# Kernel tuning notes

Hardware: AMD Instinct MI355X
Metric: run time of the kernel (lower is better)

## Reference

```python
import jax, jax.numpy as jnp
import numpy as np

N_NODES = 50000
N_EDGES = 1600000
HIDDEN = 512
LN_EPS = 1e-5


def setup_inputs() -> dict:
    key = jax.random.key(0)
    k1, k2, k3, k4 = jax.random.split(key, 4)
    label_emb = jax.random.normal(k1, (N_NODES, HIDDEN), dtype=jnp.float32)
    edge_index = jax.random.randint(k2, (2, N_EDGES), 0, N_NODES, dtype=jnp.int64)
    W = jax.random.normal(k3, (HIDDEN, HIDDEN), dtype=jnp.float32) / np.sqrt(HIDDEN)
    b = jnp.zeros((HIDDEN,), dtype=jnp.float32)
    gamma = jnp.ones((HIDDEN,), dtype=jnp.float32)
    beta = jnp.zeros((HIDDEN,), dtype=jnp.float32)
    return {"label_emb": label_emb, "edge_index": edge_index, "W": W, "b": b,
            "gamma": gamma, "beta": beta}


def _gcn_conv(x, src, dst, W, b, n_nodes):
    loops = jnp.arange(n_nodes, dtype=src.dtype)
    src_all = jnp.concatenate([src, loops])  # [E+N]
    dst_all = jnp.concatenate([dst, loops])
    ones = jnp.ones_like(dst_all, dtype=x.dtype)
    deg = jax.ops.segment_sum(ones, dst_all, num_segments=n_nodes)  # [N]
    dinv = jnp.where(deg > 0, jax.lax.rsqrt(deg), 0.0)
    norm = dinv[src_all] * dinv[dst_all]  # [E+N]
    h = x @ W  # [N, H] dense transform first (fewer FLOPs than per-edge)
    msgs = h[src_all] * norm[:, None]  # gather + per-edge scale
    out = jax.ops.segment_sum(msgs, dst_all, num_segments=n_nodes)  # scatter-add
    return out + b


def reference(label_emb, edge_index, W, b, gamma, beta):
    residual = label_emb
    src, dst = edge_index[0], edge_index[1]
    h = _gcn_conv(label_emb, src, dst, W, b, N_NODES)
    # dropout is identity at inference (training=False)
    h = residual + h
    mean = jnp.mean(h, axis=-1, keepdims=True)
    var = jnp.var(h, axis=-1, keepdims=True)
    h = (h - mean) * jax.lax.rsqrt(var + LN_EPS) * gamma + beta
    return h
```

## Files before the change

kernel.cpp:

```cpp
#include <hip/hip_runtime.h>

#define HID 512
#define CAP 128
#define BINCAP 384

typedef unsigned int uint32;
using bf16x8 = __attribute__((ext_vector_type(8))) short;
using f32x4  = __attribute__((ext_vector_type(4))) float;
using f32x2  = __attribute__((ext_vector_type(2))) float;
using u32x2  = __attribute__((ext_vector_type(2))) unsigned int;
using u32x4  = __attribute__((ext_vector_type(4))) unsigned int;
using u16x4  = __attribute__((ext_vector_type(4))) unsigned short;
using u16x8  = __attribute__((ext_vector_type(8))) unsigned short;

__device__ __forceinline__ unsigned short f2bf(float f) {
    uint32 u = __float_as_uint(f);
    uint32 r = (u + 0x7FFFu + ((u >> 16) & 1u)) >> 16;
    return (unsigned short)r;
}
__device__ __forceinline__ float bf2f(unsigned short u) {
    return __uint_as_float(((uint32)u) << 16);
}

__device__ __forceinline__ void gl_lds16(const unsigned short* g, unsigned short* l) {
    __builtin_amdgcn_global_load_lds(
        (const __attribute__((address_space(1))) void*)g,
        (__attribute__((address_space(3))) void*)l,
        16, 0, 0);
}

__global__ __launch_bounds__(256) void prep_bin(const int* __restrict__ src,
                                                const int* __restrict__ dst,
                                                int* __restrict__ bincnt,
                                                uint32* __restrict__ bins, int e,
                                                const float* __restrict__ X,
                                                unsigned short* __restrict__ Xbf,
                                                const float* __restrict__ W,
                                                unsigned short* __restrict__ Wt,
                                                int n_elems, int pad_elems,
                                                int nbb, int nbx) {
    const int bid = blockIdx.x;
    if (bid < nbb) {
        for (int i = bid * 256 + (int)threadIdx.x; i < e; i += nbb * 256) {
            int d = dst[i], s = src[i];
            int b = d >> 3;
            int p = atomicAdd(&bincnt[b], 1);
            bins[(size_t)b * BINCAP + p] = ((uint32)(d & 7) << 16) | (uint32)s;
        }
    } else if (bid < nbb + nbx) {
        int base = ((bid - nbb) * 256 + threadIdx.x) * 8;
        if (base < n_elems) {
            f32x4 a = *(const f32x4*)(X + base);
            f32x4 b = *(const f32x4*)(X + base + 4);
            u16x4 w0, w1;
            w0[0] = f2bf(a[0]); w0[1] = f2bf(a[1]); w0[2] = f2bf(a[2]); w0[3] = f2bf(a[3]);
            w1[0] = f2bf(b[0]); w1[1] = f2bf(b[1]); w1[2] = f2bf(b[2]); w1[3] = f2bf(b[3]);
            *(u16x4*)(Xbf + base) = w0;
            *(u16x4*)(Xbf + base + 4) = w1;
        } else if (base < pad_elems) {
            u16x4 z = {0, 0, 0, 0};
            *(u16x4*)(Xbf + base) = z;
            *(u16x4*)(Xbf + base + 4) = z;
        }
    } else {
        int idx = (bid - nbb - nbx) * 256 + threadIdx.x;
        if (idx < HID * HID) {
            int k = idx >> 9, n = idx & (HID - 1);
            Wt[n * HID + k] = f2bf(W[k * HID + n]);
        }
    }
}

__global__ __launch_bounds__(256) void bin2csr(const uint32* __restrict__ bins,
                                               const int* __restrict__ bincnt,
                                               unsigned short* __restrict__ csrf,
                                               int* __restrict__ fill) {
    __shared__ alignas(16) unsigned short lcs[128 * CAP];
    __shared__ int lcnt[128];
    const int b = blockIdx.x;
    for (int j = threadIdx.x; j < 128; j += 256) lcnt[j] = 0;
    __syncthreads();
    #pragma unroll
    for (int sb = 0; sb < 16; ++sb) {
        const int gb = b * 16 + sb;
        const int m = bincnt[gb];
        const uint32* be = bins + (size_t)gb * BINCAP;
        for (int i = threadIdx.x; i < m; i += 256) {
            uint32 ev = be[i];
            int ln = sb * 8 + (int)(ev >> 16);
            int p = atomicAdd(&lcnt[ln], 1);
            lcs[ln * CAP + p] = (unsigned short)(ev & 0xFFFFu);
        }
    }
    __syncthreads();
    u32x4* gout = (u32x4*)(csrf + (size_t)b * 128 * CAP);
    const u32x4* lin = (const u32x4*)lcs;
    for (int j = threadIdx.x; j < 128 * CAP / 8; j += 256) gout[j] = lin[j];
    if (threadIdx.x < 128) fill[b * 128 + threadIdx.x] = lcnt[threadIdx.x];
}

#define NWGX 4
__global__ __launch_bounds__(256) void gemm_xw(const unsigned short* __restrict__ Xbf,
                                               const unsigned short* __restrict__ Wt,
                                               const int* __restrict__ fill,
                                               unsigned char* __restrict__ hs8,
                                               int nwg) {
    __shared__ unsigned short Alds[128 * 64];
    __shared__ unsigned short Blds[128 * 64];
    const int cpx = nwg >> 3;
    const int swz = (blockIdx.x & 7) * cpx + (blockIdx.x >> 3);
    const int row_base = (swz >> 2) * 128;
    const int col_base = (swz & 3) * 128;

    const int t = threadIdx.x;
    const int lane = t & 63, wid = t >> 6;
    const int wm = wid >> 1, wn = wid & 1;

    const int srow = lane >> 3;
    const int gch  = ((lane & 7) ^ srow) * 8;
    const unsigned short* gA = Xbf + (size_t)(row_base + wid * 8 + srow) * HID + gch;
    const unsigned short* gB = Wt  + (size_t)(col_base + wid * 8 + srow) * HID + gch;
    unsigned short* lA = &Alds[wid * 512];
    unsigned short* lB = &Blds[wid * 512];

    f32x4 acc[4][4];
    #pragma unroll
    for (int m = 0; m < 4; ++m)
        #pragma unroll
        for (int n = 0; n < 4; ++n)
            acc[m][n] = (f32x4){0.f, 0.f, 0.f, 0.f};

    const int rr = lane & 15;
    const int kg8 = lane >> 4;

    for (int k0 = 0; k0 < HID; k0 += 64) {
        #pragma unroll
        for (int rd = 0; rd < 4; ++rd) {
            gl_lds16(gA + (size_t)rd * 32 * HID + k0, lA + rd * 2048);
            gl_lds16(gB + (size_t)rd * 32 * HID + k0, lB + rd * 2048);
        }
        __syncthreads();

        bf16x8 afr[4][2], bfr[4][2];
        #pragma unroll
        for (int m = 0; m < 4; ++m) {
            int row = wm * 64 + m * 16 + rr;
            #pragma unroll
            for (int ks = 0; ks < 2; ++ks)
                afr[m][ks] = *(const bf16x8*)&Alds[row * 64 + (((ks * 4 + kg8) ^ (row & 7)) * 8)];
        }
        #pragma unroll
        for (int n = 0; n < 4; ++n) {
            int row = wn * 64 + n * 16 + rr;
            #pragma unroll
            for (int ks = 0; ks < 2; ++ks)
                bfr[n][ks] = *(const bf16x8*)&Blds[row * 64 + (((ks * 4 + kg8) ^ (row & 7)) * 8)];
        }
        #pragma unroll
        for (int ks = 0; ks < 2; ++ks)
            #pragma unroll
            for (int m = 0; m < 4; ++m)
                #pragma unroll
                for (int n = 0; n < 4; ++n)
                    acc[m][n] = __builtin_amdgcn_mfma_f32_16x16x32_bf16(afr[m][ks], bfr[n][ks], acc[m][n], 0, 0, 0);
        __syncthreads();
    }

    const int rgrp = (lane >> 4) * 4;
    const int cc = lane & 15;
    #pragma unroll
    for (int m = 0; m < 4; ++m) {
        #pragma unroll
        for (int r = 0; r < 4; ++r) {
            int grow = row_base + wm * 64 + m * 16 + rgrp + r;
            float g = rsqrtf((float)fill[grow] + 1.0f);
            #pragma unroll
            for (int n = 0; n < 4; ++n) {
                int gcol = col_base + wn * 64 + n * 16 + cc;
                float v = acc[m][n][r] * g;
                unsigned int p = __builtin_amdgcn_cvt_pk_fp8_f32(v, v, 0u, false);
                hs8[(size_t)grow * HID + gcol] = (unsigned char)p;
            }
        }
    }
}

__device__ __forceinline__ void dec8(u32x2 v, float* acc) {
    f32x2 a = __builtin_amdgcn_cvt_pk_f32_fp8(v[0], false);
    f32x2 b = __builtin_amdgcn_cvt_pk_f32_fp8(v[0], true);
    f32x2 c = __builtin_amdgcn_cvt_pk_f32_fp8(v[1], false);
    f32x2 d = __builtin_amdgcn_cvt_pk_f32_fp8(v[1], true);
    acc[0] += a[0]; acc[1] += a[1]; acc[2] += b[0]; acc[3] += b[1];
    acc[4] += c[0]; acc[5] += c[1]; acc[6] += d[0]; acc[7] += d[1];
}

__global__ __launch_bounds__(256) void agg_ln(const unsigned char* __restrict__ hs8,
                                              const float* __restrict__ resid,
                                              const float* __restrict__ bvec,
                                              const float* __restrict__ gamma,
                                              const float* __restrict__ beta,
                                              const int* __restrict__ fill,
                                              const unsigned short* __restrict__ csrf,
                                              float* __restrict__ out, int nn) {
    const int wave = threadIdx.x >> 6;
    const int lane = threadIdx.x & 63;
    const int n = blockIdx.x * 4 + wave;
    if (n >= nn) return;
    const int c0 = lane * 8;

    float acc[8];
    #pragma unroll
    for (int j = 0; j < 8; ++j) acc[j] = 0.f;
    dec8(*(const u32x2*)(hs8 + (size_t)n * HID + c0), acc);

    const int m = fill[n];
    const unsigned short* idx = csrf + (size_t)n * CAP;
    int i = 0;
    for (; i + 8 <= m; i += 8) {
        u16x8 iv = *(const u16x8*)(idx + i);
        u32x2 v0 = *(const u32x2*)(hs8 + (size_t)iv[0] * HID + c0);
        u32x2 v1 = *(const u32x2*)(hs8 + (size_t)iv[1] * HID + c0);
        u32x2 v2 = *(const u32x2*)(hs8 + (size_t)iv[2] * HID + c0);
        u32x2 v3 = *(const u32x2*)(hs8 + (size_t)iv[3] * HID + c0);
        u32x2 v4 = *(const u32x2*)(hs8 + (size_t)iv[4] * HID + c0);
        u32x2 v5 = *(const u32x2*)(hs8 + (size_t)iv[5] * HID + c0);
        u32x2 v6 = *(const u32x2*)(hs8 + (size_t)iv[6] * HID + c0);
        u32x2 v7 = *(const u32x2*)(hs8 + (size_t)iv[7] * HID + c0);
        dec8(v0, acc); dec8(v1, acc); dec8(v2, acc); dec8(v3, acc);
        dec8(v4, acc); dec8(v5, acc); dec8(v6, acc); dec8(v7, acc);
    }
    for (; i < m; ++i)
        dec8(*(const u32x2*)(hs8 + (size_t)idx[i] * HID + c0), acc);

    const float g = rsqrtf((float)m + 1.0f);
    f32x4 r0 = __builtin_nontemporal_load((const f32x4*)(resid + (size_t)n * HID + c0));
    f32x4 r1 = __builtin_nontemporal_load((const f32x4*)(resid + (size_t)n * HID + c0 + 4));
    float val[8];
    #pragma unroll
    for (int j = 0; j < 4; ++j) {
        val[j]     = r0[j] + g * acc[j]     + bvec[c0 + j];
        val[j + 4] = r1[j] + g * acc[j + 4] + bvec[c0 + j + 4];
    }

    float s = 0.f, q = 0.f;
    #pragma unroll
    for (int j = 0; j < 8; ++j) { s += val[j]; q += val[j] * val[j]; }
    #pragma unroll
    for (int off = 32; off > 0; off >>= 1) {
        s += __shfl_xor(s, off, 64);
        q += __shfl_xor(q, off, 64);
    }
    const float mean = s * (1.f / 512.f);
    const float var = q * (1.f / 512.f) - mean * mean;
    const float rstd = rsqrtf(var + 1e-5f);

    f32x4 o0, o1;
    #pragma unroll
    for (int j = 0; j < 4; ++j) {
        o0[j] = (val[j]     - mean) * rstd * gamma[c0 + j]     + beta[c0 + j];
        o1[j] = (val[j + 4] - mean) * rstd * gamma[c0 + j + 4] + beta[c0 + j + 4];
    }
    __builtin_nontemporal_store(o0, (f32x4*)(out + (size_t)n * HID + c0));
    __builtin_nontemporal_store(o1, (f32x4*)(out + (size_t)n * HID + c0 + 4));
}

extern "C" void kernel_launch(void* const* d_in, const int* in_sizes, int n_in,
                              void* d_out, int out_size, void* d_ws, size_t ws_size,
                              hipStream_t stream) {
    const float* X     = (const float*)d_in[0];
    const int*   edges = (const int*)d_in[1];
    const float* W     = (const float*)d_in[2];
    const float* b     = (const float*)d_in[3];
    const float* gamma = (const float*)d_in[4];
    const float* beta  = (const float*)d_in[5];
    float* out = (float*)d_out;

    const int E = in_sizes[1] / 2;
    const int N = in_sizes[0] / HID;
    const int M_pad = ((N + 255) / 256) * 256;
    const int nslices = M_pad / 128;
    const int nbins = M_pad / 8;
    const int* src = edges;
    const int* dst = edges + E;

    char* w = (char*)d_ws;
    auto alloc = [&](size_t bytes) { char* p = w; w += (bytes + 255) & ~(size_t)255; return p; };
    int*    fill   = (int*)alloc((size_t)M_pad * 4);
    int*    bincnt = (int*)alloc((size_t)nbins * 4);
    uint32* bins   = (uint32*)alloc((size_t)nbins * BINCAP * 4);
    unsigned short* csrf = (unsigned short*)alloc((size_t)M_pad * CAP * 2);
    unsigned short* Wt   = (unsigned short*)alloc((size_t)HID * HID * 2);
    unsigned char*  hs8  = (unsigned char*)alloc((size_t)M_pad * HID);
    unsigned short* Xbf = (unsigned short*)d_out;

    hipMemsetAsync(bincnt, 0, (size_t)nbins * 4, stream);

    const int pad_elems = M_pad * HID;
    const int nbb = 2048;
    const int nbx = (pad_elems / 8 + 255) / 256;
    const int nbw = (HID * HID + 255) / 256;
    prep_bin<<<nbb + nbx + nbw, 256, 0, stream>>>(src, dst, bincnt, bins, E,
                                                  X, Xbf, W, Wt,
                                                  N * HID, pad_elems, nbb, nbx);

    bin2csr<<<nslices, 256, 0, stream>>>(bins, bincnt, csrf, fill);

    const int nwg = (M_pad / 128) * NWGX;
    gemm_xw<<<nwg, 256, 0, stream>>>(Xbf, Wt, fill, hs8, nwg);

    agg_ln<<<(N + 3) / 4, 256, 0, stream>>>(hs8, X, b, gamma, beta, fill, csrf, out, N);
}
```

Baseline: 285.6 us.

## Merge CSR build and GEMM into one launch, move source scaling to aggregation

Runs the bin-to-CSR blocks and the XW GEMM blocks in a single kernel launch, so the two independent stages can overlap and one launch gap disappears. Because the GEMM no longer waits for the degree counts, the source-side D^-1/2 scaling moves out of the GEMM epilogue. The aggregation instead multiplies each gathered row by a precomputed per-node dinv array. This adds one scalar gather per edge plus extra multiplies in the aggregation loop. It also changes fp8 quantization, since the unscaled products are now stored.

```diff
diff --git a/kernel.cpp b/kernel.cpp
--- a/kernel.cpp
+++ b/kernel.cpp
@@ -71,44 +71,53 @@
     }
 }
 
-__global__ __launch_bounds__(256) void bin2csr(const uint32* __restrict__ bins,
-                                               const int* __restrict__ bincnt,
-                                               unsigned short* __restrict__ csrf,
-                                               int* __restrict__ fill) {
-    __shared__ alignas(16) unsigned short lcs[128 * CAP];
-    __shared__ int lcnt[128];
-    const int b = blockIdx.x;
-    for (int j = threadIdx.x; j < 128; j += 256) lcnt[j] = 0;
-    __syncthreads();
-    #pragma unroll
-    for (int sb = 0; sb < 16; ++sb) {
-        const int gb = b * 16 + sb;
-        const int m = bincnt[gb];
-        const uint32* be = bins + (size_t)gb * BINCAP;
-        for (int i = threadIdx.x; i < m; i += 256) {
-            uint32 ev = be[i];
-            int ln = sb * 8 + (int)(ev >> 16);
-            int p = atomicAdd(&lcnt[ln], 1);
-            lcs[ln * CAP + p] = (unsigned short)(ev & 0xFFFFu);
-        }
-    }
-    __syncthreads();
-    u32x4* gout = (u32x4*)(csrf + (size_t)b * 128 * CAP);
-    const u32x4* lin = (const u32x4*)lcs;
-    for (int j = threadIdx.x; j < 128 * CAP / 8; j += 256) gout[j] = lin[j];
-    if (threadIdx.x < 128) fill[b * 128 + threadIdx.x] = lcnt[threadIdx.x];
-}
-
 #define NWGX 4
-__global__ __launch_bounds__(256) void gemm_xw(const unsigned short* __restrict__ Xbf,
-                                               const unsigned short* __restrict__ Wt,
-                                               const int* __restrict__ fill,
-                                               unsigned char* __restrict__ hs8,
-                                               int nwg) {
-    __shared__ unsigned short Alds[128 * 64];
-    __shared__ unsigned short Blds[128 * 64];
+__global__ __launch_bounds__(256) void csr_gemm(const uint32* __restrict__ bins,
+                                                const int* __restrict__ bincnt,
+                                                unsigned short* __restrict__ csrf,
+                                                int* __restrict__ fill,
+                                                float* __restrict__ dinvf,
+                                                const unsigned short* __restrict__ Xbf,
+                                                const unsigned short* __restrict__ Wt,
+                                                unsigned char* __restrict__ hs8,
+                                                int nslices, int nwg) {
+    __shared__ alignas(16) unsigned char smem[128 * CAP * 2 + 128 * 4];
+
+    if ((int)blockIdx.x < nslices) {
+        unsigned short* lcs = (unsigned short*)smem;
+        int* lcnt = (int*)(smem + 128 * CAP * 2);
+        const int b = blockIdx.x;
+        for (int j = threadIdx.x; j < 128; j += 256) lcnt[j] = 0;
+        __syncthreads();
+        #pragma unroll
+        for (int sb = 0; sb < 16; ++sb) {
+            const int gb = b * 16 + sb;
+            const int m = bincnt[gb];
+            const uint32* be = bins + (size_t)gb * BINCAP;
+            for (int i = threadIdx.x; i < m; i += 256) {
+                uint32 ev = be[i];
+                int ln = sb * 8 + (int)(ev >> 16);
+                int p = atomicAdd(&lcnt[ln], 1);
+                lcs[ln * CAP + p] = (unsigned short)(ev & 0xFFFFu);
+            }
+        }
+        __syncthreads();
+        u32x4* gout = (u32x4*)(csrf + (size_t)b * 128 * CAP);
+        const u32x4* lin = (const u32x4*)lcs;
+        for (int j = threadIdx.x; j < 128 * CAP / 8; j += 256) gout[j] = lin[j];
+        if (threadIdx.x < 128) {
+            int c = lcnt[threadIdx.x];
+            fill[b * 128 + threadIdx.x] = c;
+            dinvf[b * 128 + threadIdx.x] = rsqrtf((float)c + 1.0f);
+        }
+        return;
+    }
+
+    unsigned short* Alds = (unsigned short*)smem;
+    unsigned short* Blds = (unsigned short*)(smem + 128 * 64 * 2);
+    const int bx = (int)blockIdx.x - nslices;
     const int cpx = nwg >> 3;
-    const int swz = (blockIdx.x & 7) * cpx + (blockIdx.x >> 3);
+    const int swz = (bx & 7) * cpx + (bx >> 3);
     const int row_base = (swz >> 2) * 128;
     const int col_base = (swz & 3) * 128;
 
@@ -173,11 +182,10 @@
         #pragma unroll
         for (int r = 0; r < 4; ++r) {
             int grow = row_base + wm * 64 + m * 16 + rgrp + r;
-            float g = rsqrtf((float)fill[grow] + 1.0f);
             #pragma unroll
             for (int n = 0; n < 4; ++n) {
                 int gcol = col_base + wn * 64 + n * 16 + cc;
-                float v = acc[m][n][r] * g;
+                float v = acc[m][n][r];
                 unsigned int p = __builtin_amdgcn_cvt_pk_fp8_f32(v, v, 0u, false);
                 hs8[(size_t)grow * HID + gcol] = (unsigned char)p;
             }
@@ -185,13 +193,13 @@
     }
 }
 
-__device__ __forceinline__ void dec8(u32x2 v, float* acc) {
+__device__ __forceinline__ void dec8s(u32x2 v, float g, float* acc) {
     f32x2 a = __builtin_amdgcn_cvt_pk_f32_fp8(v[0], false);
     f32x2 b = __builtin_amdgcn_cvt_pk_f32_fp8(v[0], true);
     f32x2 c = __builtin_amdgcn_cvt_pk_f32_fp8(v[1], false);
     f32x2 d = __builtin_amdgcn_cvt_pk_f32_fp8(v[1], true);
-    acc[0] += a[0]; acc[1] += a[1]; acc[2] += b[0]; acc[3] += b[1];
-    acc[4] += c[0]; acc[5] += c[1]; acc[6] += d[0]; acc[7] += d[1];
+    acc[0] += g * a[0]; acc[1] += g * a[1]; acc[2] += g * b[0]; acc[3] += g * b[1];
+    acc[4] += g * c[0]; acc[5] += g * c[1]; acc[6] += g * d[0]; acc[7] += g * d[1];
 }
 
 __global__ __launch_bounds__(256) void agg_ln(const unsigned char* __restrict__ hs8,
@@ -200,6 +208,7 @@
                                               const float* __restrict__ gamma,
                                               const float* __restrict__ beta,
                                               const int* __restrict__ fill,
+                                              const float* __restrict__ dinvf,
                                               const unsigned short* __restrict__ csrf,
                                               float* __restrict__ out, int nn) {
     const int wave = threadIdx.x >> 6;
@@ -208,16 +217,19 @@
     if (n >= nn) return;
     const int c0 = lane * 8;
 
+    const float gn = dinvf[n];
     float acc[8];
     #pragma unroll
     for (int j = 0; j < 8; ++j) acc[j] = 0.f;
-    dec8(*(const u32x2*)(hs8 + (size_t)n * HID + c0), acc);
+    dec8s(*(const u32x2*)(hs8 + (size_t)n * HID + c0), gn, acc);
 
     const int m = fill[n];
     const unsigned short* idx = csrf + (size_t)n * CAP;
     int i = 0;
     for (; i + 8 <= m; i += 8) {
         u16x8 iv = *(const u16x8*)(idx + i);
+        float g0 = dinvf[iv[0]], g1 = dinvf[iv[1]], g2 = dinvf[iv[2]], g3 = dinvf[iv[3]];
+        float g4 = dinvf[iv[4]], g5 = dinvf[iv[5]], g6 = dinvf[iv[6]], g7 = dinvf[iv[7]];
         u32x2 v0 = *(const u32x2*)(hs8 + (size_t)iv[0] * HID + c0);
         u32x2 v1 = *(const u32x2*)(hs8 + (size_t)iv[1] * HID + c0);
         u32x2 v2 = *(const u32x2*)(hs8 + (size_t)iv[2] * HID + c0);
@@ -226,20 +238,21 @@
         u32x2 v5 = *(const u32x2*)(hs8 + (size_t)iv[5] * HID + c0);
         u32x2 v6 = *(const u32x2*)(hs8 + (size_t)iv[6] * HID + c0);
         u32x2 v7 = *(const u32x2*)(hs8 + (size_t)iv[7] * HID + c0);
-        dec8(v0, acc); dec8(v1, acc); dec8(v2, acc); dec8(v3, acc);
-        dec8(v4, acc); dec8(v5, acc); dec8(v6, acc); dec8(v7, acc);
-    }
-    for (; i < m; ++i)
-        dec8(*(const u32x2*)(hs8 + (size_t)idx[i] * HID + c0), acc);
-
-    const float g = rsqrtf((float)m + 1.0f);
+        dec8s(v0, g0, acc); dec8s(v1, g1, acc); dec8s(v2, g2, acc); dec8s(v3, g3, acc);
+        dec8s(v4, g4, acc); dec8s(v5, g5, acc); dec8s(v6, g6, acc); dec8s(v7, g7, acc);
+    }
+    for (; i < m; ++i) {
+        int s = idx[i];
+        dec8s(*(const u32x2*)(hs8 + (size_t)s * HID + c0), dinvf[s], acc);
+    }
+
     f32x4 r0 = __builtin_nontemporal_load((const f32x4*)(resid + (size_t)n * HID + c0));
     f32x4 r1 = __builtin_nontemporal_load((const f32x4*)(resid + (size_t)n * HID + c0 + 4));
     float val[8];
     #pragma unroll
     for (int j = 0; j < 4; ++j) {
-        val[j]     = r0[j] + g * acc[j]     + bvec[c0 + j];
-        val[j + 4] = r1[j] + g * acc[j + 4] + bvec[c0 + j + 4];
+        val[j]     = r0[j] + gn * acc[j]     + bvec[c0 + j];
+        val[j + 4] = r1[j] + gn * acc[j + 4] + bvec[c0 + j + 4];
     }
 
     float s = 0.f, q = 0.f;
@@ -286,6 +299,7 @@
     char* w = (char*)d_ws;
     auto alloc = [&](size_t bytes) { char* p = w; w += (bytes + 255) & ~(size_t)255; return p; };
     int*    fill   = (int*)alloc((size_t)M_pad * 4);
+    float*  dinvf  = (float*)alloc((size_t)M_pad * 4);
     int*    bincnt = (int*)alloc((size_t)nbins * 4);
     uint32* bins   = (uint32*)alloc((size_t)nbins * BINCAP * 4);
     unsigned short* csrf = (unsigned short*)alloc((size_t)M_pad * CAP * 2);
@@ -303,10 +317,9 @@
                                                   X, Xbf, W, Wt,
                                                   N * HID, pad_elems, nbb, nbx);
 
-    bin2csr<<<nslices, 256, 0, stream>>>(bins, bincnt, csrf, fill);
-
     const int nwg = (M_pad / 128) * NWGX;
-    gemm_xw<<<nwg, 256, 0, stream>>>(Xbf, Wt, fill, hs8, nwg);
-
-    agg_ln<<<(N + 3) / 4, 256, 0, stream>>>(hs8, X, b, gamma, beta, fill, csrf, out, N);
-}
+    csr_gemm<<<nslices + nwg, 256, 0, stream>>>(bins, bincnt, csrf, fill, dinvf,
+                                                Xbf, Wt, hs8, nslices, nwg);
+
+    agg_ln<<<(N + 3) / 4, 256, 0, stream>>>(hs8, X, b, gamma, beta, fill, dinvf, csrf, out, N);
+}
```

After: 277.1 us. -3.0%, faster.
